# Performance work log

Measured on AMD Instinct MI355X. Metric: run time of the kernel, lower is better.

The kernel has to match this reference:

```python
import jax, jax.numpy as jnp
import numpy as np

TAU = 1.0      # temperature for gumbel-softmax
EPS = 1e-12    # F.normalize eps


def _l2norm(v, axis):
    n = jnp.sqrt(jnp.sum(v * v, axis=axis, keepdims=True))
    return v / jnp.maximum(n, EPS)


def setup_inputs() -> dict:
    key = jax.random.key(0)
    k1, k2, k3, k4 = jax.random.split(key, 4)
    b, c, h, w, n = 8, 512, 64, 64, 1024
    x = jax.random.normal(k1, (b, c, h, w), dtype=jnp.float32)
    centers = jax.random.normal(k2, (n, c), dtype=jnp.float32)          # VQ codebook
    clusters = jax.random.normal(k3, (n, c), dtype=jnp.float32)         # ClusterLookup param
    gumbel_noise = jax.random.gumbel(k4, (b, n, h, w), dtype=jnp.float32)
    return {"x": x, "centers": centers, "clusters": clusters, "gumbel_noise": gumbel_noise}


def reference(x, centers, clusters, gumbel_noise):
    # similarity logits: [b, n, h, w]
    inner = jnp.einsum('bchw,nc->bnhw', x, centers)
    # hard gumbel-softmax (straight-through) over code dim
    y_soft = jax.nn.softmax((inner + gumbel_noise) / TAU, axis=1)
    idx = jnp.argmax(y_soft, axis=1)                                     # [b, h, w]
    y_hard = jax.nn.one_hot(idx, centers.shape[0], axis=1, dtype=y_soft.dtype)
    one_hot = y_hard - jax.lax.stop_gradient(y_soft) + y_soft            # [b, n, h, w]
    # quantized features: codebook lookup expressed as einsum
    z_q = jnp.einsum('bnhw,nd->bdhw', one_hot, centers)                  # [b, c, h, w]
    # ClusterLookup(z_q, alpha=None, is_direct=False)
    nf = _l2norm(z_q, axis=1)
    ncl = _l2norm(clusters, axis=1)
    ip = jnp.einsum('bchw,nc->bnhw', nf, ncl)                            # cluster logits
    preds = jnp.argmax(ip, axis=1)                                       # [b, h, w] int
    probs = jax.nn.one_hot(preds, clusters.shape[0], axis=1, dtype=ip.dtype)
    cluster_loss = -jnp.mean(jnp.sum(probs * ip, axis=1))
    return (cluster_loss, preds, ip, z_q)
```

## Files before the change

kernel.cpp:

```cpp
#include <hip/hip_runtime.h>
#include <math.h>

#define C 512
#define HW 4096
#define N 1024
#define NPIX 32768
#define MARGIN 2.0f

typedef short s16x8 __attribute__((ext_vector_type(8)));
typedef float f32x4 __attribute__((ext_vector_type(4)));

__device__ inline unsigned short f2bf(float f) {
    unsigned int u = __float_as_uint(f);
    return (unsigned short)((u + 0x7FFFu + ((u >> 16) & 1u)) >> 16);
}
__device__ inline float h2f(unsigned short u) {
    _Float16 h; __builtin_memcpy(&h, &u, 2); return (float)h;
}
__device__ inline unsigned short f2h(float f) {
    _Float16 h = (_Float16)f; unsigned short u; __builtin_memcpy(&u, &h, 2); return u;
}
__device__ inline unsigned int mono(float v) {
    unsigned int u = __float_as_uint(v);
    return (u & 0x80000000u) ? ~u : (u | 0x80000000u);
}
__device__ inline void gload_lds16(const void* gsrc, void* ldst) {
    __builtin_amdgcn_global_load_lds(
        (const __attribute__((address_space(1))) unsigned int*)gsrc,
        (__attribute__((address_space(3))) unsigned int*)ldst, 16, 0, 0);
}

__global__ __launch_bounds__(64) void k_norms(const float* __restrict__ centers,
                                              const float* __restrict__ clusters,
                                              float* __restrict__ cnorm,
                                              float* __restrict__ clnorm) {
    int r = blockIdx.x;
    const float* src = (r < N) ? (centers + (size_t)r * C) : (clusters + (size_t)(r - N) * C);
    int lane = threadIdx.x;
    float s = 0.f;
    for (int k = lane; k < C; k += 64) { float v = src[k]; s += v * v; }
    #pragma unroll
    for (int m = 1; m < 64; m <<= 1) s += __shfl_xor(s, m, 64);
    if (lane == 0) {
        float nrm = sqrtf(s);
        if (nrm < 1e-12f) nrm = 1e-12f;
        if (r < N) cnorm[r] = nrm; else clnorm[r - N] = nrm;
    }
}

__global__ __launch_bounds__(256) void k_gemmM(const float* __restrict__ centers,
                                               const float* __restrict__ clusters,
                                               const float* __restrict__ cnorm,
                                               const float* __restrict__ clnorm,
                                               float* __restrict__ M) {
    __shared__ float as[32][68];
    __shared__ float bs[32][68];
    int tid = threadIdx.x;
    int tx = tid & 15, ty = tid >> 4;
    int i0 = blockIdx.x * 64, j0 = blockIdx.y * 64;
    int lrow = tid >> 2, lkq = (tid & 3) * 8;
    float acc[4][4] = {};
    for (int kc = 0; kc < C; kc += 32) {
        float4 a0 = *(const float4*)(centers + (size_t)(i0 + lrow) * C + kc + lkq);
        float4 a1 = *(const float4*)(centers + (size_t)(i0 + lrow) * C + kc + lkq + 4);
        float4 b0 = *(const float4*)(clusters + (size_t)(j0 + lrow) * C + kc + lkq);
        float4 b1 = *(const float4*)(clusters + (size_t)(j0 + lrow) * C + kc + lkq + 4);
        __syncthreads();
        as[lkq+0][lrow]=a0.x; as[lkq+1][lrow]=a0.y; as[lkq+2][lrow]=a0.z; as[lkq+3][lrow]=a0.w;
        as[lkq+4][lrow]=a1.x; as[lkq+5][lrow]=a1.y; as[lkq+6][lrow]=a1.z; as[lkq+7][lrow]=a1.w;
        bs[lkq+0][lrow]=b0.x; bs[lkq+1][lrow]=b0.y; bs[lkq+2][lrow]=b0.z; bs[lkq+3][lrow]=b0.w;
        bs[lkq+4][lrow]=b1.x; bs[lkq+5][lrow]=b1.y; bs[lkq+6][lrow]=b1.z; bs[lkq+7][lrow]=b1.w;
        __syncthreads();
        #pragma unroll
        for (int k = 0; k < 32; k += 4) {
            float av[4][4], bv[4][4];
            #pragma unroll
            for (int kk = 0; kk < 4; ++kk) {
                float4 ta = *(const float4*)&as[k+kk][tx*4];
                float4 tb = *(const float4*)&bs[k+kk][ty*4];
                av[kk][0]=ta.x; av[kk][1]=ta.y; av[kk][2]=ta.z; av[kk][3]=ta.w;
                bv[kk][0]=tb.x; bv[kk][1]=tb.y; bv[kk][2]=tb.z; bv[kk][3]=tb.w;
            }
            #pragma unroll
            for (int kk = 0; kk < 4; ++kk)
                #pragma unroll
                for (int ii = 0; ii < 4; ++ii)
                    #pragma unroll
                    for (int jj = 0; jj < 4; ++jj)
                        acc[ii][jj] = fmaf(av[kk][ii], bv[kk][jj], acc[ii][jj]);
        }
    }
    float rci[4], rcj[4];
    #pragma unroll
    for (int ii = 0; ii < 4; ++ii) rci[ii] = cnorm[i0 + tx*4 + ii];
    #pragma unroll
    for (int jj = 0; jj < 4; ++jj) rcj[jj] = clnorm[j0 + ty*4 + jj];
    #pragma unroll
    for (int ii = 0; ii < 4; ++ii)
        #pragma unroll
        for (int jj = 0; jj < 4; ++jj)
            M[(size_t)(i0 + tx*4 + ii) * N + (j0 + ty*4 + jj)] = acc[ii][jj] / (rci[ii] * rcj[jj]);
}

__global__ __launch_bounds__(256) void k_rowstat(const float* __restrict__ M,
                                                 float* __restrict__ rowmax,
                                                 int* __restrict__ rowarg) {
    __shared__ float sv[256];
    __shared__ int   sa[256];
    int i = blockIdx.x, tid = threadIdx.x;
    float bv = -INFINITY; int ba = 0;
    for (int j = tid; j < N; j += 256) {
        float v = M[(size_t)i * N + j];
        if (v > bv || (v == bv && j < ba)) { bv = v; ba = j; }
    }
    sv[tid] = bv; sa[tid] = ba;
    __syncthreads();
    for (int s = 128; s > 0; s >>= 1) {
        if (tid < s) {
            float v = sv[tid + s]; int a = sa[tid + s];
            if (v > sv[tid] || (v == sv[tid] && a < sa[tid])) { sv[tid] = v; sa[tid] = a; }
        }
        __syncthreads();
    }
    if (tid == 0) { rowmax[i] = sv[0]; rowarg[i] = sa[0]; }
}

__global__ __launch_bounds__(256) void k_prepT(const float* __restrict__ x,
                                               float* __restrict__ xT) {
    __shared__ float t[64][65];
    int bidx = blockIdx.x;
    int pt = bidx & 63, kt = (bidx >> 6) & 7, b = bidx >> 9;
    int r = threadIdx.x >> 4, c4 = (threadIdx.x & 15) * 4;
    const float* src = x + ((size_t)b * C + kt * 64) * HW + pt * 64;
    #pragma unroll
    for (int rr = 0; rr < 4; ++rr) {
        int row = rr * 16 + r;
        float4 v = *(const float4*)(src + (size_t)row * HW + c4);
        t[row][c4] = v.x; t[row][c4+1] = v.y; t[row][c4+2] = v.z; t[row][c4+3] = v.w;
    }
    __syncthreads();
    float* dst = xT + ((size_t)b * HW + pt * 64) * C + kt * 64;
    #pragma unroll
    for (int rr = 0; rr < 4; ++rr) {
        int row = rr * 16 + r;
        float4 v = { t[c4][row], t[c4+1][row], t[c4+2][row], t[c4+3][row] };
        *(float4*)(dst + (size_t)row * C + c4) = v;
    }
}

__global__ __launch_bounds__(64) void k_cenfrag(const float* __restrict__ centers,
                                                unsigned short* __restrict__ cenB) {
    int f = blockIdx.x;
    int nt = f >> 4, kt = f & 15;
    int lane = threadIdx.x;
    int r = lane & 15, g = lane >> 4;
    const float* src = centers + (size_t)(nt * 16 + r) * C + kt * 32 + g * 4;
    float4 lo = *(const float4*)src;
    float4 hi = *(const float4*)(src + 16);
    union { unsigned short us[8]; uint4 q; } u;
    u.us[0]=f2bf(lo.x); u.us[1]=f2bf(lo.y); u.us[2]=f2bf(lo.z); u.us[3]=f2bf(lo.w);
    u.us[4]=f2bf(hi.x); u.us[5]=f2bf(hi.y); u.us[6]=f2bf(hi.z); u.us[7]=f2bf(hi.w);
    *(uint4*)(cenB + ((size_t)f * 64 + lane) * 8) = u.q;
}

__global__ __launch_bounds__(256, 2) void k_fused(const float* __restrict__ xT,
                                                  const unsigned short* __restrict__ cenB,
                                                  const float* __restrict__ gumbel,
                                                  const float* __restrict__ centers,
                                                  int* __restrict__ idxb) {
    __shared__ unsigned short cen[3][8192];
    __shared__ float glds[3][1024];
    __shared__ unsigned long long pixkey[64];
    __shared__ unsigned int candlist[4][256];
    __shared__ int candcount[4];

    int tid = threadIdx.x;
    int lane = tid & 63, w = tid >> 6;
    int r = lane & 15, g = lane >> 4;

    int p0 = blockIdx.x * 64;
    int b = p0 >> 12, hw0 = p0 & (HW - 1);

    if (tid < 64) pixkey[tid] = 0ull;
    if (tid < 4) candcount[tid] = 0;

    s16x8 a[16];
    {
        const float* xrow = xT + (size_t)(p0 + w * 16 + r) * C;
        #pragma unroll
        for (int kt = 0; kt < 16; ++kt) {
            float4 lo = *(const float4*)(xrow + kt * 32 + g * 4);
            float4 hi = *(const float4*)(xrow + kt * 32 + 16 + g * 4);
            s16x8 t;
            t[0]=(short)f2bf(lo.x); t[1]=(short)f2bf(lo.y); t[2]=(short)f2bf(lo.z); t[3]=(short)f2bf(lo.w);
            t[4]=(short)f2bf(hi.x); t[5]=(short)f2bf(hi.y); t[6]=(short)f2bf(hi.z); t[7]=(short)f2bf(hi.w);
            a[kt] = t;
        }
    }

    int grow_ = tid >> 4;
    int gcol_ = ((tid ^ (tid >> 4)) & 15) * 4;
    const float* gbase = gumbel + (size_t)b * N * HW + hw0 + gcol_;

    #define STAGE(T, BUF) { \
        const char* s_ = (const char*)cenB + (size_t)(T) * 16384 + w * 4096 + lane * 16; \
        char* d_ = (char*)&cen[0][0] + (BUF) * 16384 + w * 4096; \
        gload_lds16(s_, d_); gload_lds16(s_ + 1024, d_ + 1024); \
        gload_lds16(s_ + 2048, d_ + 2048); gload_lds16(s_ + 3072, d_ + 3072); \
        gload_lds16(gbase + (size_t)((T) * 16 + grow_) * HW, \
                    (char*)&glds[0][0] + (BUF) * 4096 + tid * 16); \
    }

    __builtin_amdgcn_sched_barrier(0);
    STAGE(0, 0);
    STAGE(1, 1);
    __builtin_amdgcn_sched_barrier(0);
    asm volatile("s_waitcnt vmcnt(5)" ::: "memory");
    __builtin_amdgcn_s_barrier();
    __builtin_amdgcn_sched_barrier(0);

    float m4[4] = {-INFINITY, -INFINITY, -INFINITY, -INFINITY};
    int c0 = 0;
    int gswz = r * 64 + ((((w << 2) + g) ^ r) << 2);

    for (int tc = 0; tc < 8; ++tc) {
        unsigned int keepH[16];
        #pragma unroll
        for (int s = 0; s < 8; ++s) {
            int t = tc * 8 + s;
            const s16x8* bp = (const s16x8*)((char*)&cen[0][0] + c0 * 16384) + lane;
            f32x4 acc0 = {0.f,0.f,0.f,0.f}, acc1 = {0.f,0.f,0.f,0.f};
            #pragma unroll
            for (int kt = 0; kt < 16; kt += 2) {
                acc0 = __builtin_amdgcn_mfma_f32_16x16x32_bf16(a[kt],   bp[kt*64],     acc0, 0,0,0);
                acc1 = __builtin_amdgcn_mfma_f32_16x16x32_bf16(a[kt+1], bp[(kt+1)*64], acc1, 0,0,0);
            }
            f32x4 gv = *(const f32x4*)((const float*)&glds[0][0] + c0 * 1024 + gswz);
            float v0 = acc0[0]+acc1[0]+gv[0], v1 = acc0[1]+acc1[1]+gv[1];
            float v2 = acc0[2]+acc1[2]+gv[2], v3 = acc0[3]+acc1[3]+gv[3];
            m4[0]=fmaxf(m4[0],v0); m4[1]=fmaxf(m4[1],v1);
            m4[2]=fmaxf(m4[2],v2); m4[3]=fmaxf(m4[3],v3);
            keepH[s*2]   = (unsigned int)f2h(v0) | ((unsigned int)f2h(v1) << 16);
            keepH[s*2+1] = (unsigned int)f2h(v2) | ((unsigned int)f2h(v3) << 16);
            asm volatile("s_waitcnt lgkmcnt(0)" ::: "memory");
            __builtin_amdgcn_sched_barrier(0);
            __builtin_amdgcn_s_barrier();
            __builtin_amdgcn_sched_barrier(0);
            int c2 = c0 + 2; if (c2 >= 3) c2 -= 3;
            if (t + 2 <= 63) { STAGE(t + 2, c2); }
            __builtin_amdgcn_sched_barrier(0);
            if (t + 2 <= 63)      { asm volatile("s_waitcnt vmcnt(5)" ::: "memory"); }
            else if (t + 1 <= 63) { asm volatile("s_waitcnt vmcnt(0)" ::: "memory"); }
            __builtin_amdgcn_s_barrier();
            __builtin_amdgcn_sched_barrier(0);
            c0 = c0 + 1; if (c0 >= 3) c0 -= 3;
        }
        #pragma unroll
        for (int s2 = 1; s2 < 16; s2 <<= 1) {
            #pragma unroll
            for (int j = 0; j < 4; ++j) m4[j] = fmaxf(m4[j], __shfl_xor(m4[j], s2, 64));
        }
        float thr[4];
        #pragma unroll
        for (int j = 0; j < 4; ++j) thr[j] = m4[j] - MARGIN;
        #pragma unroll
        for (int s = 0; s < 8; ++s) {
            int nn = ((tc * 8 + s) << 4) + r;
            #pragma unroll
            for (int j2 = 0; j2 < 2; ++j2) {
                unsigned int pk = keepH[s * 2 + j2];
                float lo = h2f((unsigned short)(pk & 0xFFFFu));
                float hi = h2f((unsigned short)(pk >> 16));
                if (lo >= thr[j2 * 2]) {
                    int pos = atomicAdd(&candcount[w], 1);
                    if (pos < 256) candlist[w][pos] =
                        (unsigned int)nn | ((unsigned int)(w * 16 + g * 4 + j2 * 2) << 10);
                }
                if (hi >= thr[j2 * 2 + 1]) {
                    int pos = atomicAdd(&candcount[w], 1);
                    if (pos < 256) candlist[w][pos] =
                        (unsigned int)nn | ((unsigned int)(w * 16 + g * 4 + j2 * 2 + 1) << 10);
                }
            }
        }
    }
    #undef STAGE

    int cc = candcount[w]; if (cc > 256) cc = 256;
    int sl = lane & 15, cg = lane >> 4;
    for (int t0 = 0; t0 < cc; t0 += 4) {
        int c = t0 + cg;
        bool valid = c < cc;
        unsigned int e = candlist[w][valid ? c : 0];
        int n = (int)(e & 1023u), pl = (int)(e >> 10);
        const float* xr = xT + (size_t)(p0 + pl) * C;
        const float* cenr = centers + (size_t)n * C;
        float s = 0.f;
        #pragma unroll
        for (int m = 0; m < 8; ++m) {
            int G = sl + (m << 4);
            float4 xv = *(const float4*)(xr + (G << 2));
            float4 cv = *(const float4*)(cenr + (G << 2));
            s = fmaf(xv.x, cv.x, s); s = fmaf(xv.y, cv.y, s);
            s = fmaf(xv.z, cv.z, s); s = fmaf(xv.w, cv.w, s);
        }
        #pragma unroll
        for (int s2 = 1; s2 < 16; s2 <<= 1) s += __shfl_xor(s, s2, 64);
        if (valid && sl == 0) {
            float val = s + gumbel[((size_t)b * N + n) * HW + hw0 + pl];
            unsigned long long key = ((unsigned long long)mono(val) << 32) | (unsigned int)(1023 - n);
            atomicMax(&pixkey[pl], key);
        }
    }
    __syncthreads();
    if (tid < 64) idxb[p0 + tid] = 1023 - (int)(unsigned int)(pixkey[tid] & 0xFFFFFFFFull);
}

__global__ __launch_bounds__(256) void k_preds(const int* __restrict__ idxb,
                                               const float* __restrict__ rowmax,
                                               const int* __restrict__ rowarg,
                                               float* __restrict__ preds_out,
                                               float* __restrict__ partial) {
    __shared__ float sv[256];
    int gid = blockIdx.x * 256 + threadIdx.x;
    int i = idxb[gid];
    preds_out[gid] = (float)rowarg[i];
    sv[threadIdx.x] = rowmax[i];
    __syncthreads();
    for (int s = 128; s > 0; s >>= 1) {
        if (threadIdx.x < s) sv[threadIdx.x] += sv[threadIdx.x + s];
        __syncthreads();
    }
    if (threadIdx.x == 0) partial[blockIdx.x] = sv[0];
}

__global__ __launch_bounds__(256) void k_gather(const float* __restrict__ src, int ncols,
                                                const int* __restrict__ idx,
                                                float* __restrict__ dst) {
    __shared__ float rows[64][65];
    int tile = blockIdx.x;
    int col0 = blockIdx.y * 64;
    int tid = threadIdx.x;
    int lane = tid & 63, w = tid >> 6;
    int b = tile >> 6, hw0 = (tile & 63) << 6;
    #pragma unroll
    for (int r8 = 0; r8 < 16; ++r8) {
        int r = w * 16 + r8;
        int row = idx[tile * 64 + r];
        rows[r][lane] = src[(size_t)row * ncols + col0 + lane];
    }
    __syncthreads();
    #pragma unroll
    for (int jj = 0; jj < 16; ++jj) {
        int j = col0 + w * 16 + jj;
        dst[((size_t)b * ncols + j) * HW + hw0 + lane] = rows[lane][w * 16 + jj];
    }
}

__global__ __launch_bounds__(128) void k_loss(const float* __restrict__ partial,
                                              float* __restrict__ out) {
    __shared__ float sv[128];
    sv[threadIdx.x] = partial[threadIdx.x];
    __syncthreads();
    for (int s = 64; s > 0; s >>= 1) {
        if (threadIdx.x < s) sv[threadIdx.x] += sv[threadIdx.x + s];
        __syncthreads();
    }
    if (threadIdx.x == 0) out[0] = -(sv[0] / 32768.0f);
}

extern "C" void kernel_launch(void* const* d_in, const int* in_sizes, int n_in,
                              void* d_out, int out_size, void* d_ws, size_t ws_size,
                              hipStream_t stream) {
    const float* x        = (const float*)d_in[0];
    const float* centers  = (const float*)d_in[1];
    const float* clusters = (const float*)d_in[2];
    const float* gumbel   = (const float*)d_in[3];
    float* out = (float*)d_out;

    char* w = (char*)d_ws;
    int*   idxb    = (int*)w;
    float* cnorm   = (float*)(w + 131072);
    float* clnorm  = cnorm + 1024;
    float* rowmax  = clnorm + 1024;
    int*   rowarg  = (int*)(rowmax + 1024);
    float* partial = (float*)(rowarg + 1024);
    float* M       = (float*)(w + 262144);
    unsigned short* cenB = (unsigned short*)(w + 4456448);

    float* out_loss  = out;
    float* out_preds = out + 1;
    float* out_ip    = out + 1 + 32768;
    float* out_zq    = out + 1 + 32768 + (size_t)N * NPIX;

    float* xT = out_zq;

    k_norms  <<<2048, 64, 0, stream>>>(centers, clusters, cnorm, clnorm);
    k_gemmM  <<<dim3(16, 16), 256, 0, stream>>>(centers, clusters, cnorm, clnorm, M);
    k_rowstat<<<1024, 256, 0, stream>>>(M, rowmax, rowarg);
    k_cenfrag<<<1024, 64, 0, stream>>>(centers, cenB);
    k_prepT  <<<4096, 256, 0, stream>>>(x, xT);
    k_fused  <<<512, 256, 0, stream>>>(xT, cenB, gumbel, centers, idxb);
    k_preds  <<<128, 256, 0, stream>>>(idxb, rowmax, rowarg, out_preds, partial);
    k_gather <<<dim3(512, 16), 256, 0, stream>>>(M, N, idxb, out_ip);
    k_gather <<<dim3(512, 8),  256, 0, stream>>>(centers, C, idxb, out_zq);
    k_loss   <<<1, 128, 0, stream>>>(partial, out_loss);
}
```

Before: 257.5 us.

## Deepen fused-kernel prefetch to 4 stages and enlarge transpose/gather tiles

The fused GEMM/argmax kernel now keeps the gumbel values in registers instead of staging them through LDS, and uses a 4-deep codebook buffer with a barrier-per-tile schedule so loads are issued three tiles ahead. The transpose kernel moves to 128x128 tiles and the gather kernel handles 256 pixels per block, giving fewer, larger blocks. The deeper prefetch is meant to hide global latency behind the MFMAs, but it costs more LDS and registers, which may limit occupancy. The larger tiles in the other kernels cut the number of blocks and may reduce parallelism.

After: 278.7 us. 8.2% more time.

```diff
diff --git a/kernel.cpp b/kernel.cpp
--- a/kernel.cpp
+++ b/kernel.cpp
@@ -127,22 +127,22 @@
 
 __global__ __launch_bounds__(256) void k_prepT(const float* __restrict__ x,
                                                float* __restrict__ xT) {
-    __shared__ float t[64][65];
+    __shared__ float t[128][129];
     int bidx = blockIdx.x;
-    int pt = bidx & 63, kt = (bidx >> 6) & 7, b = bidx >> 9;
-    int r = threadIdx.x >> 4, c4 = (threadIdx.x & 15) * 4;
-    const float* src = x + ((size_t)b * C + kt * 64) * HW + pt * 64;
-    #pragma unroll
-    for (int rr = 0; rr < 4; ++rr) {
-        int row = rr * 16 + r;
+    int pt = bidx & 31, kt = (bidx >> 5) & 3, b = bidx >> 7;
+    int r0 = threadIdx.x >> 5, c4 = (threadIdx.x & 31) * 4;
+    const float* src = x + ((size_t)b * C + kt * 128) * HW + pt * 128;
+    #pragma unroll
+    for (int rr = 0; rr < 16; ++rr) {
+        int row = rr * 8 + r0;
         float4 v = *(const float4*)(src + (size_t)row * HW + c4);
         t[row][c4] = v.x; t[row][c4+1] = v.y; t[row][c4+2] = v.z; t[row][c4+3] = v.w;
     }
     __syncthreads();
-    float* dst = xT + ((size_t)b * HW + pt * 64) * C + kt * 64;
-    #pragma unroll
-    for (int rr = 0; rr < 4; ++rr) {
-        int row = rr * 16 + r;
+    float* dst = xT + ((size_t)b * HW + pt * 128) * C + kt * 128;
+    #pragma unroll
+    for (int rr = 0; rr < 16; ++rr) {
+        int row = rr * 8 + r0;
         float4 v = { t[c4][row], t[c4+1][row], t[c4+2][row], t[c4+3][row] };
         *(float4*)(dst + (size_t)row * C + c4) = v;
     }
@@ -163,13 +163,29 @@
     *(uint4*)(cenB + ((size_t)f * 64 + lane) * 8) = u.q;
 }
 
+__device__ inline void mfma_tile(const s16x8* a, const unsigned short* cenbuf, int lane,
+                                 f32x4 gv, float* m4, unsigned int* kh) {
+    const s16x8* bp = (const s16x8*)cenbuf + lane;
+    f32x4 acc0 = {0.f,0.f,0.f,0.f}, acc1 = {0.f,0.f,0.f,0.f};
+    #pragma unroll
+    for (int kt = 0; kt < 16; kt += 2) {
+        acc0 = __builtin_amdgcn_mfma_f32_16x16x32_bf16(a[kt],   bp[kt*64],     acc0, 0,0,0);
+        acc1 = __builtin_amdgcn_mfma_f32_16x16x32_bf16(a[kt+1], bp[(kt+1)*64], acc1, 0,0,0);
+    }
+    float v0 = acc0[0]+acc1[0]+gv[0], v1 = acc0[1]+acc1[1]+gv[1];
+    float v2 = acc0[2]+acc1[2]+gv[2], v3 = acc0[3]+acc1[3]+gv[3];
+    m4[0] = fmaxf(m4[0], v0); m4[1] = fmaxf(m4[1], v1);
+    m4[2] = fmaxf(m4[2], v2); m4[3] = fmaxf(m4[3], v3);
+    kh[0] = (unsigned int)f2h(v0) | ((unsigned int)f2h(v1) << 16);
+    kh[1] = (unsigned int)f2h(v2) | ((unsigned int)f2h(v3) << 16);
+}
+
 __global__ __launch_bounds__(256, 2) void k_fused(const float* __restrict__ xT,
                                                   const unsigned short* __restrict__ cenB,
                                                   const float* __restrict__ gumbel,
                                                   const float* __restrict__ centers,
                                                   int* __restrict__ idxb) {
-    __shared__ unsigned short cen[3][8192];
-    __shared__ float glds[3][1024];
+    __shared__ unsigned short cen[4][8192];
     __shared__ unsigned long long pixkey[64];
     __shared__ unsigned int candlist[4][256];
     __shared__ int candcount[4];
@@ -197,94 +213,97 @@
             a[kt] = t;
         }
     }
-
-    int grow_ = tid >> 4;
-    int gcol_ = ((tid ^ (tid >> 4)) & 15) * 4;
-    const float* gbase = gumbel + (size_t)b * N * HW + hw0 + gcol_;
-
-    #define STAGE(T, BUF) { \
+    const float* gpx = gumbel + (size_t)b * N * HW + hw0 + w * 16 + g * 4;
+    f32x4 gvp[4];
+
+    #define STAGE_CEN(T, BUF) { \
         const char* s_ = (const char*)cenB + (size_t)(T) * 16384 + w * 4096 + lane * 16; \
-        char* d_ = (char*)&cen[0][0] + (BUF) * 16384 + w * 4096; \
+        char* d_ = (char*)&cen[BUF][0] + w * 4096; \
         gload_lds16(s_, d_); gload_lds16(s_ + 1024, d_ + 1024); \
-        gload_lds16(s_ + 2048, d_ + 2048); gload_lds16(s_ + 3072, d_ + 3072); \
-        gload_lds16(gbase + (size_t)((T) * 16 + grow_) * HW, \
-                    (char*)&glds[0][0] + (BUF) * 4096 + tid * 16); \
-    }
-
+        gload_lds16(s_ + 2048, d_ + 2048); gload_lds16(s_ + 3072, d_ + 3072); }
+    #define LOAD_GV(T, SLOT) gvp[SLOT] = *(const f32x4*)(gpx + (size_t)((T) * 16 + r) * HW);
+
+    asm volatile("s_waitcnt vmcnt(0)" ::: "memory");
     __builtin_amdgcn_sched_barrier(0);
-    STAGE(0, 0);
-    STAGE(1, 1);
+    STAGE_CEN(0, 0); LOAD_GV(0, 0);
+    STAGE_CEN(1, 1); LOAD_GV(1, 1);
+    STAGE_CEN(2, 2); LOAD_GV(2, 2);
     __builtin_amdgcn_sched_barrier(0);
-    asm volatile("s_waitcnt vmcnt(5)" ::: "memory");
+    asm volatile("s_waitcnt vmcnt(10)" ::: "memory");
     __builtin_amdgcn_s_barrier();
     __builtin_amdgcn_sched_barrier(0);
 
     float m4[4] = {-INFINITY, -INFINITY, -INFINITY, -INFINITY};
-    int c0 = 0;
-    int gswz = r * 64 + ((((w << 2) + g) ^ r) << 2);
-
-    for (int tc = 0; tc < 8; ++tc) {
+
+    #define SCAN_CHUNK(TCB, KH) { \
+        _Pragma("unroll") \
+        for (int s2 = 1; s2 < 16; s2 <<= 1) { \
+            _Pragma("unroll") \
+            for (int j = 0; j < 4; ++j) m4[j] = fmaxf(m4[j], __shfl_xor(m4[j], s2, 64)); \
+        } \
+        float thr[4]; \
+        _Pragma("unroll") \
+        for (int j = 0; j < 4; ++j) thr[j] = m4[j] - MARGIN; \
+        _Pragma("unroll") \
+        for (int s = 0; s < 8; ++s) { \
+            int nn = (((TCB) * 8 + s) << 4) + r; \
+            _Pragma("unroll") \
+            for (int j2 = 0; j2 < 2; ++j2) { \
+                unsigned int pk = (KH)[s * 2 + j2]; \
+                float lo = h2f((unsigned short)(pk & 0xFFFFu)); \
+                float hi = h2f((unsigned short)(pk >> 16)); \
+                if (lo >= thr[j2 * 2]) { \
+                    int pos = atomicAdd(&candcount[w], 1); \
+                    if (pos < 256) candlist[w][pos] = \
+                        (unsigned int)nn | ((unsigned int)(w * 16 + g * 4 + j2 * 2) << 10); \
+                } \
+                if (hi >= thr[j2 * 2 + 1]) { \
+                    int pos = atomicAdd(&candcount[w], 1); \
+                    if (pos < 256) candlist[w][pos] = \
+                        (unsigned int)nn | ((unsigned int)(w * 16 + g * 4 + j2 * 2 + 1) << 10); \
+                } \
+            } \
+        } }
+
+    for (int tc = 0; tc < 7; ++tc) {
         unsigned int keepH[16];
         #pragma unroll
         for (int s = 0; s < 8; ++s) {
             int t = tc * 8 + s;
-            const s16x8* bp = (const s16x8*)((char*)&cen[0][0] + c0 * 16384) + lane;
-            f32x4 acc0 = {0.f,0.f,0.f,0.f}, acc1 = {0.f,0.f,0.f,0.f};
-            #pragma unroll
-            for (int kt = 0; kt < 16; kt += 2) {
-                acc0 = __builtin_amdgcn_mfma_f32_16x16x32_bf16(a[kt],   bp[kt*64],     acc0, 0,0,0);
-                acc1 = __builtin_amdgcn_mfma_f32_16x16x32_bf16(a[kt+1], bp[(kt+1)*64], acc1, 0,0,0);
+            STAGE_CEN(t + 3, (s + 3) & 3);
+            LOAD_GV(t + 3, (s + 3) & 3);
+            __builtin_amdgcn_sched_barrier(0);
+            mfma_tile(a, &cen[s & 3][0], lane, gvp[s & 3], m4, &keepH[s * 2]);
+            __builtin_amdgcn_sched_barrier(0);
+            asm volatile("s_waitcnt vmcnt(10) lgkmcnt(0)" ::: "memory");
+            __builtin_amdgcn_s_barrier();
+            __builtin_amdgcn_sched_barrier(0);
+        }
+        SCAN_CHUNK(tc, keepH);
+    }
+    {
+        unsigned int keepH[16];
+        #pragma unroll
+        for (int s = 0; s < 8; ++s) {
+            int t = 56 + s;
+            if (s <= 4) {
+                STAGE_CEN(t + 3, (s + 3) & 3);
+                LOAD_GV(t + 3, (s + 3) & 3);
             }
-            f32x4 gv = *(const f32x4*)((const float*)&glds[0][0] + c0 * 1024 + gswz);
-            float v0 = acc0[0]+acc1[0]+gv[0], v1 = acc0[1]+acc1[1]+gv[1];
-            float v2 = acc0[2]+acc1[2]+gv[2], v3 = acc0[3]+acc1[3]+gv[3];
-            m4[0]=fmaxf(m4[0],v0); m4[1]=fmaxf(m4[1],v1);
-            m4[2]=fmaxf(m4[2],v2); m4[3]=fmaxf(m4[3],v3);
-            keepH[s*2]   = (unsigned int)f2h(v0) | ((unsigned int)f2h(v1) << 16);
-            keepH[s*2+1] = (unsigned int)f2h(v2) | ((unsigned int)f2h(v3) << 16);
-            asm volatile("s_waitcnt lgkmcnt(0)" ::: "memory");
-            __builtin_amdgcn_sched_barrier(0);
-            __builtin_amdgcn_s_barrier();
-            __builtin_amdgcn_sched_barrier(0);
-            int c2 = c0 + 2; if (c2 >= 3) c2 -= 3;
-            if (t + 2 <= 63) { STAGE(t + 2, c2); }
-            __builtin_amdgcn_sched_barrier(0);
-            if (t + 2 <= 63)      { asm volatile("s_waitcnt vmcnt(5)" ::: "memory"); }
-            else if (t + 1 <= 63) { asm volatile("s_waitcnt vmcnt(0)" ::: "memory"); }
-            __builtin_amdgcn_s_barrier();
-            __builtin_amdgcn_sched_barrier(0);
-            c0 = c0 + 1; if (c0 >= 3) c0 -= 3;
-        }
-        #pragma unroll
-        for (int s2 = 1; s2 < 16; s2 <<= 1) {
-            #pragma unroll
-            for (int j = 0; j < 4; ++j) m4[j] = fmaxf(m4[j], __shfl_xor(m4[j], s2, 64));
-        }
-        float thr[4];
-        #pragma unroll
-        for (int j = 0; j < 4; ++j) thr[j] = m4[j] - MARGIN;
-        #pragma unroll
-        for (int s = 0; s < 8; ++s) {
-            int nn = ((tc * 8 + s) << 4) + r;
-            #pragma unroll
-            for (int j2 = 0; j2 < 2; ++j2) {
-                unsigned int pk = keepH[s * 2 + j2];
-                float lo = h2f((unsigned short)(pk & 0xFFFFu));
-                float hi = h2f((unsigned short)(pk >> 16));
-                if (lo >= thr[j2 * 2]) {
-                    int pos = atomicAdd(&candcount[w], 1);
-                    if (pos < 256) candlist[w][pos] =
-                        (unsigned int)nn | ((unsigned int)(w * 16 + g * 4 + j2 * 2) << 10);
-                }
-                if (hi >= thr[j2 * 2 + 1]) {
-                    int pos = atomicAdd(&candcount[w], 1);
-                    if (pos < 256) candlist[w][pos] =
-                        (unsigned int)nn | ((unsigned int)(w * 16 + g * 4 + j2 * 2 + 1) << 10);
-                }
-            }
-        }
-    }
-    #undef STAGE
+            __builtin_amdgcn_sched_barrier(0);
+            mfma_tile(a, &cen[s & 3][0], lane, gvp[s & 3], m4, &keepH[s * 2]);
+            __builtin_amdgcn_sched_barrier(0);
+            if (s <= 4)      { asm volatile("s_waitcnt vmcnt(10) lgkmcnt(0)" ::: "memory"); }
+            else if (s == 5) { asm volatile("s_waitcnt vmcnt(5) lgkmcnt(0)" ::: "memory"); }
+            else if (s == 6) { asm volatile("s_waitcnt vmcnt(0) lgkmcnt(0)" ::: "memory"); }
+            if (s < 7) { __builtin_amdgcn_s_barrier(); }
+            __builtin_amdgcn_sched_barrier(0);
+        }
+        SCAN_CHUNK(7, keepH);
+    }
+    #undef STAGE_CEN
+    #undef LOAD_GV
+    #undef SCAN_CHUNK
 
     int cc = candcount[w]; if (cc > 256) cc = 256;
     int sl = lane & 15, cg = lane >> 4;
@@ -337,23 +356,25 @@
 __global__ __launch_bounds__(256) void k_gather(const float* __restrict__ src, int ncols,
                                                 const int* __restrict__ idx,
                                                 float* __restrict__ dst) {
-    __shared__ float rows[64][65];
+    __shared__ float rows[256][65];
     int tile = blockIdx.x;
     int col0 = blockIdx.y * 64;
     int tid = threadIdx.x;
     int lane = tid & 63, w = tid >> 6;
-    int b = tile >> 6, hw0 = (tile & 63) << 6;
-    #pragma unroll
-    for (int r8 = 0; r8 < 16; ++r8) {
-        int r = w * 16 + r8;
-        int row = idx[tile * 64 + r];
-        rows[r][lane] = src[(size_t)row * ncols + col0 + lane];
+    int p0 = tile * 256;
+    int b = p0 >> 12, hw0 = p0 & (HW - 1);
+    for (int r8 = 0; r8 < 64; ++r8) {
+        int rrow = w * 64 + r8;
+        int row = idx[p0 + rrow];
+        rows[rrow][lane] = src[(size_t)row * ncols + col0 + lane];
     }
     __syncthreads();
     #pragma unroll
     for (int jj = 0; jj < 16; ++jj) {
         int j = col0 + w * 16 + jj;
-        dst[((size_t)b * ncols + j) * HW + hw0 + lane] = rows[lane][w * 16 + jj];
+        #pragma unroll
+        for (int q = 0; q < 4; ++q)
+            dst[((size_t)b * ncols + j) * HW + hw0 + q * 64 + lane] = rows[q * 64 + lane][w * 16 + jj];
     }
 }
 
@@ -399,10 +420,10 @@
     k_gemmM  <<<dim3(16, 16), 256, 0, stream>>>(centers, clusters, cnorm, clnorm, M);
     k_rowstat<<<1024, 256, 0, stream>>>(M, rowmax, rowarg);
     k_cenfrag<<<1024, 64, 0, stream>>>(centers, cenB);
-    k_prepT  <<<4096, 256, 0, stream>>>(x, xT);
+    k_prepT  <<<1024, 256, 0, stream>>>(x, xT);
     k_fused  <<<512, 256, 0, stream>>>(xT, cenB, gumbel, centers, idxb);
     k_preds  <<<128, 256, 0, stream>>>(idxb, rowmax, rowarg, out_preds, partial);
-    k_gather <<<dim3(512, 16), 256, 0, stream>>>(M, N, idxb, out_ip);
-    k_gather <<<dim3(512, 8),  256, 0, stream>>>(centers, C, idxb, out_zq);
+    k_gather <<<dim3(128, 16), 256, 0, stream>>>(M, N, idxb, out_ip);
+    k_gather <<<dim3(128, 8),  256, 0, stream>>>(centers, C, idxb, out_zq);
     k_loss   <<<1, 128, 0, stream>>>(partial, out_loss);
 }
```
